# Kernel optimization log

Measured on AMD Instinct MI355X. Metric: run time of the kernel, lower is better.

Reference implementation:

```python
import jax, jax.numpy as jnp
import numpy as np


def setup_inputs() -> dict:
    key = jax.random.key(0)
    x = jax.random.normal(key, (64, 3, 224, 224), dtype=jnp.float32)
    return {"x": x, "patch_size": 16, "overlap": 8}


def reference(x, patch_size, overlap):
    # x: [B, C, H, H]
    B, C, H, _ = x.shape
    stride = patch_size - overlap
    assert (H - patch_size) % stride == 0, 'adjust the patch_size and the overlap_size!'
    n = (H - patch_size) // stride + 1  # patch_num per spatial dim
    # window row/col indices: [n, p]
    idx = jnp.arange(n)[:, None] * stride + jnp.arange(patch_size)[None, :]
    # gather rows then cols in one vectorized pass (no Python loop over patches)
    rows = x[:, :, idx, :]            # [B, C, n, p, H]
    patches = rows[:, :, :, :, idx]   # [B, C, n, p, n, p]
    # b c h d1 w d2 -> b h w c d1 d2
    patches = patches.transpose(0, 2, 4, 1, 3, 5)
    # b h w c d1 d2 -> b (h w) c (d1 d2)
    return patches.reshape(B, n * n, C, patch_size * patch_size)
```

## Files before the change

kernel.cpp:

```cpp
#include <hip/hip_runtime.h>


constexpr int NB  = 64;
constexpr int NC  = 3;
constexpr int HWD = 224;
constexpr int PS  = 16;
constexpr int ST  = 8;
constexpr int NP  = 27;
constexpr int ROW4 = HWD / 4;
constexpr int LDSW = 228;
constexpr int TPB  = 256;

__global__ __launch_bounds__(TPB) void overlap_patch_lds(
    const float4* __restrict__ x, float4* __restrict__ out)
{
    const int blk = blockIdx.x;
    const int c   = blk % NC;
    const int tmp = blk / NC;
    const int py  = tmp % NP;
    const int b   = tmp / NP;

    __shared__ float lds[PS * LDSW];

    const int t = threadIdx.x;

    const int gbase = ((b * NC + c) * HWD + py * ST) * ROW4;
    #pragma unroll
    for (int k = 0; k < 4; ++k) {
        const int j = t + k * TPB;
        if (j < PS * ROW4) {
            const int r    = j / ROW4;
            const int col4 = j - r * ROW4;
            const float4 v = x[gbase + j];
            *(float4*)&lds[r * LDSW + col4 * 4] = v;
        }
    }
    __syncthreads();

    const int obase = ((b * NP * NP + py * NP) * NC + c) * 64;
    #pragma unroll
    for (int k = 0; k < 7; ++k) {
        const int j = t + k * TPB;
        if (j < NP * 64) {
            const int px = j >> 6;
            const int q4 = j & 63;
            const int r  = q4 >> 2;
            const int s  = (q4 & 3) << 2;
            const float4 v = *(const float4*)&lds[r * LDSW + px * ST + s];
            out[obase + px * (NC * 64) + q4] = v;
        }
    }
}

extern "C" void kernel_launch(void* const* d_in, const int* in_sizes, int n_in,
                              void* d_out, int out_size, void* d_ws, size_t ws_size,
                              hipStream_t stream) {
    const float4* x = (const float4*)d_in[0];
    float4* out = (float4*)d_out;
    const int grid = NB * NP * NC;
    overlap_patch_lds<<<grid, TPB, 0, stream>>>(x, out);
}
```

Before: 173.8 us.

## Merge channels per block for contiguous output writes and use nontemporal stores

Each block now handles all three channels of one patch row, so the output region it writes (27 patches x 3 channels x 256 floats) is one fully contiguous span instead of three strided pieces. Block size doubles to 512 and LDS triples to hold all channels. Output stores use nontemporal hints to avoid polluting cache with write-once data. The grid is a third the size, which may reduce parallelism, and the larger LDS footprint may lower occupancy.

```diff
diff --git a/kernel.cpp b/kernel.cpp
--- a/kernel.cpp
+++ b/kernel.cpp
@@ -1,5 +1,7 @@
 #include <hip/hip_runtime.h>
 
+
+typedef float nfloat4 __attribute__((ext_vector_type(4)));
 
 constexpr int NB  = 64;
 constexpr int NC  = 3;
@@ -9,45 +11,47 @@
 constexpr int NP  = 27;
 constexpr int ROW4 = HWD / 4;
 constexpr int LDSW = 228;
-constexpr int TPB  = 256;
+constexpr int TPB  = 512;
+constexpr int NLOAD4  = NC * PS * ROW4;
+constexpr int NSTORE4 = NP * NC * 64;
 
-__global__ __launch_bounds__(TPB) void overlap_patch_lds(
-    const float4* __restrict__ x, float4* __restrict__ out)
+__global__ __launch_bounds__(TPB) void overlap_patch_seq(
+    const nfloat4* __restrict__ x, nfloat4* __restrict__ out)
 {
-    const int blk = blockIdx.x;
-    const int c   = blk % NC;
-    const int tmp = blk / NC;
-    const int py  = tmp % NP;
-    const int b   = tmp / NP;
+    const int py = blockIdx.x % NP;
+    const int b  = blockIdx.x / NP;
 
-    __shared__ float lds[PS * LDSW];
+    __shared__ float lds[NC * PS * LDSW];
 
     const int t = threadIdx.x;
 
-    const int gbase = ((b * NC + c) * HWD + py * ST) * ROW4;
     #pragma unroll
-    for (int k = 0; k < 4; ++k) {
+    for (int k = 0; k < 6; ++k) {
         const int j = t + k * TPB;
-        if (j < PS * ROW4) {
-            const int r    = j / ROW4;
-            const int col4 = j - r * ROW4;
-            const float4 v = x[gbase + j];
-            *(float4*)&lds[r * LDSW + col4 * 4] = v;
+        if (j < NLOAD4) {
+            const int c    = j / (PS * ROW4);
+            const int rem  = j - c * (PS * ROW4);
+            const int r    = rem / ROW4;
+            const int col4 = rem - r * ROW4;
+            const nfloat4 v = x[((b * NC + c) * HWD + py * ST + r) * ROW4 + col4];
+            *(nfloat4*)&lds[(c * PS + r) * LDSW + col4 * 4] = v;
         }
     }
     __syncthreads();
 
-    const int obase = ((b * NP * NP + py * NP) * NC + c) * 64;
+    const long obase = (long)(b * NP * NP + py * NP) * (NC * 64);
     #pragma unroll
-    for (int k = 0; k < 7; ++k) {
+    for (int k = 0; k < 11; ++k) {
         const int j = t + k * TPB;
-        if (j < NP * 64) {
-            const int px = j >> 6;
-            const int q4 = j & 63;
-            const int r  = q4 >> 2;
-            const int s  = (q4 & 3) << 2;
-            const float4 v = *(const float4*)&lds[r * LDSW + px * ST + s];
-            out[obase + px * (NC * 64) + q4] = v;
+        if (j < NSTORE4) {
+            const int px  = j / (NC * 64);
+            const int rem = j - px * (NC * 64);
+            const int c   = rem >> 6;
+            const int q4  = rem & 63;
+            const int r   = q4 >> 2;
+            const int s   = (q4 & 3) << 2;
+            const nfloat4 v = *(const nfloat4*)&lds[(c * PS + r) * LDSW + px * ST + s];
+            __builtin_nontemporal_store(v, &out[obase + j]);
         }
     }
 }
@@ -55,8 +59,8 @@
 extern "C" void kernel_launch(void* const* d_in, const int* in_sizes, int n_in,
                               void* d_out, int out_size, void* d_ws, size_t ws_size,
                               hipStream_t stream) {
-    const float4* x = (const float4*)d_in[0];
-    float4* out = (float4*)d_out;
-    const int grid = NB * NP * NC;
-    overlap_patch_lds<<<grid, TPB, 0, stream>>>(x, out);
+    const nfloat4* x = (const nfloat4*)d_in[0];
+    nfloat4* out = (nfloat4*)d_out;
+    const int grid = NB * NP;
+    overlap_patch_seq<<<grid, TPB, 0, stream>>>(x, out);
 }
```

Result: no change. 177.0 us (+1.8%).
